# Optimization experiments

Measured on AMD Instinct MI355X. Metric: run time of the kernel, lower is better.

Reference implementation:

```python
import jax, jax.numpy as jnp
import numpy as np
import math

B, DM, H, W = 2, 96, 64, 64
DI, N, R, K = 192, 16, 6, 8


def _ln(x, w, b):
    mu = jnp.mean(x, axis=-1, keepdims=True)
    var = jnp.var(x, axis=-1, keepdims=True)
    return (x - mu) / jnp.sqrt(var + 1e-5) * w + b


def _conv2d(x, w, b, groups=1):
    y = jax.lax.conv_general_dilated(x, w, (1, 1), 'SAME',
                                     dimension_numbers=('NCHW', 'OIHW', 'NCHW'),
                                     feature_group_count=groups)
    return y + b[None, :, None, None]


def setup_inputs() -> dict:
    key = jax.random.key(0)
    ks = jax.random.split(key, 16)
    f32 = jnp.float32
    rn = lambda k, s, sc=0.02: jax.random.normal(k, s, dtype=f32) * sc
    dt = jnp.exp(jax.random.uniform(ks[11], (K, DI), dtype=f32)
                 * (math.log(0.1) - math.log(0.001)) + math.log(0.001))
    dt_bias = dt + jnp.log(-jnp.expm1(-dt))  # inverse softplus
    return dict(
        feat_m1=jax.random.normal(ks[0], (B, DM, H, W), f32),
        feat_m2=jax.random.normal(ks[1], (B, DM, H, W), f32),
        ln1_w=jnp.ones(DM, f32), ln1_b=jnp.zeros(DM, f32),
        ln2_w=jnp.ones(DM, f32), ln2_b=jnp.zeros(DM, f32),
        in_proj_m1_w=rn(ks[2], (2 * DI, DM)),
        in_proj_m2_w=rn(ks[3], (2 * DI, DM)),
        conv_m1_w=rn(ks[4], (DI, 1, 3, 3), 0.1), conv_m1_b=jnp.zeros(DI, f32),
        conv_m2_w=rn(ks[5], (DI, 1, 3, 3), 0.1), conv_m2_b=jnp.zeros(DI, f32),
        x_proj_weight=rn(ks[6], (K, R + 2 * N, DI)),
        dt_projs_weight=rn(ks[7], (K, DI, R), R ** -0.5),
        dt_projs_bias=dt_bias,
        A_logs=jnp.log(jnp.tile(jnp.arange(1, N + 1, dtype=f32)[None], (K * DI, 1))),
        Ds=jnp.ones(K * DI, f32),
        out_norm_w=jnp.ones(DI, f32), out_norm_b=jnp.zeros(DI, f32),
        cc0_w=rn(ks[8], (DI, 2, 3, 3), 0.1), cc0_b=jnp.zeros(DI, f32),
        cc1_w=rn(ks[9], (DI, 1, 3, 3), 0.1), cc1_b=jnp.zeros(DI, f32),
        cc2_w=rn(ks[10], (DM, DI, 1, 1), 0.05), cc2_b=jnp.zeros(DM, f32),
    )


def reference(feat_m1, feat_m2, ln1_w, ln1_b, ln2_w, ln2_b,
              in_proj_m1_w, in_proj_m2_w, conv_m1_w, conv_m1_b,
              conv_m2_w, conv_m2_b, x_proj_weight, dt_projs_weight,
              dt_projs_bias, A_logs, Ds, out_norm_w, out_norm_b,
              cc0_w, cc0_b, cc1_w, cc1_b, cc2_w, cc2_b):
    silu = jax.nn.silu
    Bb, _, Hh, Ww = feat_m1.shape
    L = Hh * Ww

    def branch(feat, lw, lb, pw, cw, cb):
        f = _ln(feat.transpose(0, 2, 3, 1), lw, lb)        # [B,H,W,DM]
        xz = f @ pw.T                                      # [B,H,W,2*DI]
        x, z = jnp.split(xz, 2, axis=-1)
        z = silu(z.transpose(0, 3, 1, 2))                  # [B,DI,H,W]
        x = silu(_conv2d(x.transpose(0, 3, 1, 2), cw, cb, groups=cw.shape[0]))
        return x, z

    x1, z1 = branch(feat_m1, ln1_w, ln1_b, in_proj_m1_w, conv_m1_w, conv_m1_b)
    x2, z2 = branch(feat_m2, ln2_w, ln2_b, in_proj_m2_w, conv_m2_w, conv_m2_b)
    Di = x1.shape[1]

    # 4 directions x 2 modalities -> K=8 scan streams
    x_hwwh = jnp.stack([x1.reshape(Bb, Di, L), x2.reshape(Bb, Di, L),
                        x1.transpose(0, 1, 3, 2).reshape(Bb, Di, L),
                        x2.transpose(0, 1, 3, 2).reshape(Bb, Di, L)], axis=1)
    xs = jnp.concatenate([x_hwwh, jnp.flip(x_hwwh, axis=-1)], axis=1)  # [B,K,DI,L]
    Kk = xs.shape[1]

    x_dbl = jnp.einsum('bkdl,kcd->bkcl', xs, x_proj_weight)
    Rr, Nn = dt_projs_weight.shape[2], A_logs.shape[1]
    dts, Bs, Cs = jnp.split(x_dbl, [Rr, Rr + Nn], axis=2)
    dts = jnp.einsum('bkrl,kdr->bkdl', dts, dt_projs_weight)

    A = -jnp.exp(A_logs).reshape(Kk, Di, Nn)               # [K,DI,N]
    delta = jax.nn.softplus(dts + dt_projs_bias[None, :, :, None])

    us = jnp.moveaxis(xs, -1, 0)      # [L,B,K,DI]
    ds = jnp.moveaxis(delta, -1, 0)   # [L,B,K,DI]
    bs = jnp.moveaxis(Bs, -1, 0)      # [L,B,K,N]
    cs = jnp.moveaxis(Cs, -1, 0)      # [L,B,K,N]

    def step(h, inp):
        u_t, d_t, b_t, c_t = inp
        h = jnp.exp(d_t[..., None] * A) * h + (d_t * u_t)[..., None] * b_t[:, :, None, :]
        return h, jnp.einsum('bkdn,bkn->bkd', h, c_t)

    h0 = jnp.zeros((Bb, Kk, Di, Nn), xs.dtype)
    _, ys = jax.lax.scan(step, h0, (us, ds, bs, cs))
    out_y = jnp.moveaxis(ys, 0, -1) + Ds.reshape(Kk, Di)[None, :, :, None] * xs  # [B,K,DI,L]

    inv_y = jnp.flip(out_y[:, 4:], axis=-1)

    def wh(t):  # undo transposed raster order
        return t.reshape(Bb, 2, Di, Ww, Hh).transpose(0, 1, 2, 4, 3).reshape(Bb, 2, Di, L)

    wh_y = wh(out_y[:, 2:4])
    invwh_y = wh(inv_y[:, 2:4])
    y = (out_y[:, 0] + inv_y[:, 0] + wh_y[:, 0] + invwh_y[:, 0]
         + out_y[:, 1] + inv_y[:, 1] + wh_y[:, 1] + invwh_y[:, 1])  # [B,DI,L]

    y = _ln(y.transpose(0, 2, 1), out_norm_w, out_norm_b).reshape(Bb, Hh, Ww, Di)
    yc = y.transpose(0, 3, 1, 2)
    y_fus = jnp.concatenate([yc * z1, yc * z2], axis=1)    # [B,2*DI,H,W]
    y_fus = silu(_conv2d(y_fus, cc0_w, cc0_b, groups=Di))
    y_fus = silu(_conv2d(y_fus, cc1_w, cc1_b, groups=Di))
    y_fus = _conv2d(y_fus, cc2_w, cc2_b, groups=1)
    return y_fus + feat_m1 + feat_m2
```

## Files before the change

### kernel.cpp

```cpp
#include <hip/hip_runtime.h>
#include <math.h>

#define Bq 2
#define DMq 96
#define Lq 4096
#define DIq 192
#define Nq 16
#define Rq 6
#define Kq 8
#define Cq 38
#define NCH 128
#define CHL 32

typedef _Float16 f16x2 __attribute__((ext_vector_type(2)));

#if defined(__has_builtin)
#if __has_builtin(__builtin_amdgcn_fdot2)
#define HAVE_FDOT2 1
#endif
#endif

__device__ __forceinline__ float fdot2_(f16x2 a, f16x2 b, float c) {
#ifdef HAVE_FDOT2
  return __builtin_amdgcn_fdot2(a, b, c, false);
#else
  return c + (float)a.x * (float)b.x + (float)a.y * (float)b.y;
#endif
}

__device__ __forceinline__ f16x2 pkrtz(float a, float b) {
#if defined(__has_builtin) && __has_builtin(__builtin_amdgcn_cvt_pkrtz)
  auto r = __builtin_amdgcn_cvt_pkrtz(a, b);
  return *(f16x2*)&r;
#else
  return (f16x2){(_Float16)a, (_Float16)b};
#endif
}

__device__ __forceinline__ f16x2 u2h(unsigned u) {
  union { unsigned u; f16x2 h; } v; v.u = u; return v.h;
}
__device__ __forceinline__ unsigned h2u(f16x2 h) {
  union { unsigned u; f16x2 h; } v; v.h = h; return v.u;
}

__device__ __forceinline__ float sigmoidf_(float x) { return 1.f / (1.f + __expf(-x)); }

__global__ __launch_bounds__(256) void kprep(
    const float* __restrict__ pw1, const float* __restrict__ pw2,
    const float* __restrict__ ln1w, const float* __restrict__ ln1b,
    const float* __restrict__ ln2w, const float* __restrict__ ln2b,
    const float* __restrict__ xpw, const float* __restrict__ w2,
    _Float16* __restrict__ pw1h, _Float16* __restrict__ pw2h,
    _Float16* __restrict__ xpwh, _Float16* __restrict__ w2h,
    float* __restrict__ PQ) {
  int r = blockIdx.x * 256 + threadIdx.x;
  if (r < 768) {
    int br = r >= 384;
    int c = r - br * 384;
    const float* pw = br ? pw2 : pw1;
    const float* lw = br ? ln2w : ln1w;
    const float* lb = br ? ln2b : ln1b;
    _Float16* dst = br ? pw2h : pw1h;
    float P = 0.f, Q = 0.f;
    for (int cc = 0; cc < DMq; ++cc) {
      float w = pw[c * DMq + cc];
      P += w * lb[cc];
      Q += w * lw[cc];
      dst[c * DMq + cc] = (_Float16)(w * lw[cc]);
    }
    PQ[br * 768 + 2 * c] = P;
    PQ[br * 768 + 2 * c + 1] = Q;
  } else if (r < 768 + 304) {
    int rr = r - 768;
    for (int d = 0; d < DIq; ++d) xpwh[rr * DIq + d] = (_Float16)xpw[rr * DIq + d];
  } else if (r < 768 + 304 + 96) {
    int rr = r - 1072;
    for (int d = 0; d < DIq; ++d) w2h[rr * DIq + d] = (_Float16)w2[rr * DIq + d];
  }
}

__global__ __launch_bounds__(512, 2) void k1_branch(
    const float* __restrict__ feat1, const float* __restrict__ feat2,
    const _Float16* __restrict__ pw1h, const _Float16* __restrict__ pw2h,
    const float* __restrict__ PQ,
    _Float16* __restrict__ xpre1, _Float16* __restrict__ xpre2,
    _Float16* __restrict__ z1, _Float16* __restrict__ z2) {
  int blk = blockIdx.x;
  int cq = blk & 1;
  int tile = (blk >> 1) & 63;
  int b = (blk >> 7) & 1;
  int br = blk >> 8;
  int l0 = tile * 64;
  const float* feat = br ? feat2 : feat1;
  const f16x2* pwh = (const f16x2*)(br ? pw2h : pw1h);
  const float* pq = PQ + br * 768;
  _Float16* xpre = br ? xpre2 : xpre1;
  _Float16* zsil = br ? z2 : z1;
  int lane = threadIdx.x & 63;
  int wid = __builtin_amdgcn_readfirstlane(threadIdx.x >> 6);
  const float* fp = feat + (size_t)b * DMq * Lq + l0 + lane;
  f16x2 fr2[48];
  float s = 0.f, s2 = 0.f;
#pragma unroll
  for (int i = 0; i < 48; ++i) {
    float v0 = fp[(size_t)(2 * i) * Lq];
    float v1 = fp[(size_t)(2 * i + 1) * Lq];
    s += v0 + v1;
    s2 += v0 * v0 + v1 * v1;
    fr2[i] = (f16x2){(_Float16)v0, (_Float16)v1};
  }
  float mu = s * (1.f / DMq);
  float var = s2 * (1.f / DMq) - mu * mu;
  float rs = rsqrtf(var + 1e-5f);
  int cbase = cq * 192 + wid * 24;
  for (int g = 0; g < 6; ++g) {
    int c = cbase + g * 4;
    const f16x2* w0 = pwh + (size_t)c * 48;
    float a0 = 0.f, a1 = 0.f, a2 = 0.f, a3 = 0.f;
#pragma unroll
    for (int i = 0; i < 48; ++i) {
      f16x2 v = fr2[i];
      a0 = fdot2_(v, w0[i], a0);
      a1 = fdot2_(v, w0[48 + i], a1);
      a2 = fdot2_(v, w0[96 + i], a2);
      a3 = fdot2_(v, w0[144 + i], a3);
    }
    float acc[4] = {a0, a1, a2, a3};
#pragma unroll
    for (int q = 0; q < 4; ++q) {
      int c2 = c + q;
      float out = rs * acc[q] - rs * mu * pq[2 * c2 + 1] + pq[2 * c2];
      if (c2 < DIq) {
        xpre[(size_t)(b * DIq + c2) * Lq + l0 + lane] = (_Float16)out;
      } else {
        zsil[(size_t)(b * DIq + (c2 - DIq)) * Lq + l0 + lane] =
            (_Float16)(out * sigmoidf_(out));
      }
    }
  }
}

__global__ __launch_bounds__(256) void k2_dwconv(
    const _Float16* __restrict__ xpre1, const _Float16* __restrict__ xpre2,
    const float* __restrict__ cw1, const float* __restrict__ cb1,
    const float* __restrict__ cw2, const float* __restrict__ cb2,
    _Float16* __restrict__ xsh) {
  int blk = blockIdx.x;
  int mod = blk >= 384;
  int r = blk - mod * 384;
  int strip = r & 31;
  int dg = (r >> 5) % 6;
  int b = r / 192;
  const _Float16* xpre = mod ? xpre2 : xpre1;
  const float* cw = mod ? cw2 : cw1;
  const float* cb = mod ? cb2 : cb1;
  int d0 = dg * 32;
  int h0 = strip * 2;
  __shared__ float in_s[4][64][33];
  int tid = threadIdx.x;
  const _Float16* src = xpre + (size_t)(b * DIq + d0) * Lq;
  for (int i = tid; i < 4 * 64 * 32; i += 256) {
    int w = i & 63;
    int t = i >> 6;
    int dd = t & 31;
    int rr = t >> 5;
    int row = h0 + rr - 1;
    float v = 0.f;
    if (row >= 0 && row < 64) v = (float)src[(size_t)dd * Lq + row * 64 + w];
    in_s[rr][w][dd] = v;
  }
  __syncthreads();
  int dd = tid & 31;
  float w9[9];
#pragma unroll
  for (int i = 0; i < 9; i++) w9[i] = cw[(d0 + dd) * 9 + i];
  float bias = cb[d0 + dd];
  _Float16* dst = xsh + (size_t)(b * 2 + mod) * Lq * DIq + d0 + dd;
  for (int i = tid; i < 2 * 64 * 32; i += 256) {
    int w = (i >> 5) & 63;
    int hh = i >> 11;
    float acc = bias;
#pragma unroll
    for (int dh = 0; dh < 3; dh++) {
#pragma unroll
      for (int dw = 0; dw < 3; dw++) {
        int ww = w + dw - 1;
        if (ww < 0 || ww > 63) continue;
        acc += in_s[hh + dh][ww][dd] * w9[dh * 3 + dw];
      }
    }
    float v = acc * sigmoidf_(acc);
    dst[((size_t)(h0 + hh) * 64 + w) * DIq] = (_Float16)v;
  }
}

__global__ __launch_bounds__(512, 2) void k3_proj(
    const _Float16* __restrict__ xsh, const _Float16* __restrict__ xpwh,
    unsigned* __restrict__ dtBu, unsigned* __restrict__ Ccu) {
  int blk = blockIdx.x;
  int tile = blk & 63;
  int kp = (blk >> 6) & 3;
  int b = blk >> 8;
  int mod = kp & 1;
  bool tr = kp >= 2;
  int tid = threadIdx.x;
  int lane = tid & 63;
  int wid = __builtin_amdgcn_readfirstlane(tid >> 6);
  int halfk = wid >> 2;
  int chq = wid & 3;
  int kk = kp + halfk * 4;
  int chb = chq * 10;
  __shared__ unsigned osu[2][64][25];
  if (chq == 0) { osu[halfk][lane][6] = 0u; osu[halfk][lane][7] = 0u; }
  int p = tr ? (lane * 64 + tile) : (tile * 64 + lane);
  const _Float16* xp = xsh + (size_t)(b * 2 + mod) * Lq * DIq + (size_t)p * DIq;
  float acc[10];
#pragma unroll
  for (int g = 0; g < 10; ++g) acc[g] = 0.f;
  for (int chunk = 0; chunk < 2; ++chunk) {
    f16x2 fr2[48];
    const uint4* xq = (const uint4*)(xp + chunk * 96);
#pragma unroll
    for (int i = 0; i < 12; ++i) {
      uint4 v = xq[i];
      fr2[4 * i] = u2h(v.x); fr2[4 * i + 1] = u2h(v.y);
      fr2[4 * i + 2] = u2h(v.z); fr2[4 * i + 3] = u2h(v.w);
    }
#pragma unroll
    for (int g = 0; g < 10; ++g) {
      int c = chb + g;
      int cr = (c <= 37) ? c : 37;
      const f16x2* w0 = (const f16x2*)(xpwh + ((size_t)kk * Cq + cr) * DIq) + chunk * 48;
      float a = acc[g];
#pragma unroll
      for (int i = 0; i < 48; ++i) a = fdot2_(fr2[i], w0[i], a);
      acc[g] = a;
    }
  }
#pragma unroll
  for (int g = 0; g < 10; g += 2) {
    int c = chb + g;
    if (c >= Cq) break;
    if (c < 6) {
      osu[halfk][lane][c] = __float_as_uint(acc[g]);
      osu[halfk][lane][c + 1] = __float_as_uint(acc[g + 1]);
    } else {
      int word = (c < 22) ? (8 + ((c - 6) >> 1)) : (16 + ((c - 22) >> 1));
      f16x2 pk = pkrtz(acc[g], acc[g + 1]);
      osu[halfk][lane][word] = h2u(pk);
    }
  }
  __syncthreads();
  for (int i = tid; i < 2 * 64 * 16; i += 512) {
    int hk = i >> 10;
    int rem = i & 1023;
    int jr = rem >> 4, slot = rem & 15;
    int kk2 = kp + hk * 4;
    int l = hk ? (4095 - tile * 64 - jr) : (tile * 64 + jr);
    dtBu[((size_t)(b * Kq + kk2) * Lq + l) * 16 + slot] = osu[hk][jr][slot];
  }
  for (int i = tid; i < 2 * 64 * 8; i += 512) {
    int hk = i >> 9;
    int rem = i & 511;
    int jr = rem >> 3, slot = rem & 7;
    int kk2 = kp + hk * 4;
    int l = hk ? (4095 - tile * 64 - jr) : (tile * 64 + jr);
    Ccu[((size_t)(b * Kq + kk2) * Lq + l) * 8 + slot] = osu[hk][jr][16 + slot];
  }
}

#define PREAMBLE(Q0, Q1, U)                                               \
  float a = bias + __uint_as_float(Q0.x) * wr[0] +                        \
            __uint_as_float(Q0.y) * wr[1] + __uint_as_float(Q0.z) * wr[2] + \
            __uint_as_float(Q0.w) * wr[3] + __uint_as_float(Q1.x) * wr[4] + \
            __uint_as_float(Q1.y) * wr[5];                                \
  float E_ = __expf(-fabsf(a));                                           \
  float dt = fmaxf(a, 0.f) + __logf(1.f + E_);                            \
  float du = dt * (U);                                                    \
  float e1f = __expf(-dt);                                                \
  float e2f = e1f * e1f;                                                  \
  f16x2 P1 = pkrtz(e1f, e2f);                                             \
  f16x2 Dp = pkrtz(e2f, e2f);                                             \
  f16x2 du2 = pkrtz(du, du);                                              \
  f16x2 pe1 = P1 * Dp, pe2 = pe1 * Dp, pe3 = pe2 * Dp, pe4 = pe3 * Dp,   \
        pe5 = pe4 * Dp, pe6 = pe5 * Dp, pe7 = pe6 * Dp;

#define HUPDATE(Q2, Q3)                                                   \
  hp0 = P1 * hp0 + du2 * u2h(Q2.x); hp1 = pe1 * hp1 + du2 * u2h(Q2.y);    \
  hp2 = pe2 * hp2 + du2 * u2h(Q2.z); hp3 = pe3 * hp3 + du2 * u2h(Q2.w);   \
  hp4 = pe4 * hp4 + du2 * u2h(Q3.x); hp5 = pe5 * hp5 + du2 * u2h(Q3.y);   \
  hp6 = pe6 * hp6 + du2 * u2h(Q3.z); hp7 = pe7 * hp7 + du2 * u2h(Q3.w);

#define STEPA(Q0, Q1, Q2, Q3, U) {                                        \
  PREAMBLE(Q0, Q1, U)                                                     \
  sdt += dt;                                                              \
  HUPDATE(Q2, Q3) }

#define STEPC(Q0, Q1, Q2, Q3, Q4, Q5, U, J) {                             \
  PREAMBLE(Q0, Q1, U)                                                     \
  HUPDATE(Q2, Q3)                                                         \
  float yv = 0.f;                                                         \
  yv = fdot2_(hp0, u2h(Q4.x), yv); yv = fdot2_(hp1, u2h(Q4.y), yv);       \
  yv = fdot2_(hp2, u2h(Q4.z), yv); yv = fdot2_(hp3, u2h(Q4.w), yv);       \
  yv = fdot2_(hp4, u2h(Q5.x), yv); yv = fdot2_(hp5, u2h(Q5.y), yv);       \
  yv = fdot2_(hp6, u2h(Q5.z), yv); yv = fdot2_(hp7, u2h(Q5.w), yv);       \
  yp[(size_t)(J) * DIq] = (_Float16)(yv + Dv * (U)); }

#define LD4(pfx, J) { const uint4* _q = sp + (size_t)(J) * 4;             \
  pfx##0 = _q[0]; pfx##1 = _q[1]; pfx##2 = _q[2]; pfx##3 = _q[3]; }

#define LD6C(pfx, J) { const uint4* _q = sp + (size_t)(J) * 4;            \
  pfx##0 = _q[0]; pfx##1 = _q[1]; pfx##2 = _q[2]; pfx##3 = _q[3];         \
  const uint4* _c = cp + (size_t)(J) * 2;                                 \
  pfx##4 = _c[0]; pfx##5 = _c[1]; }

__device__ __forceinline__ int canonpos_(int l, bool rev, bool tr) {
  int q = rev ? 4095 - l : l;
  return tr ? (((q & 63) << 6) | (q >> 6)) : q;
}

__global__ __launch_bounds__(192, 6) void k4a_local(
    const _Float16* __restrict__ xsh, const unsigned* __restrict__ dtBu,
    const float* __restrict__ dtw, const float* __restrict__ dtb,
    float* __restrict__ sumdt, _Float16* __restrict__ hendh) {
  int blk = blockIdx.x;
  int c = blk & 127, k = (blk >> 7) & 7, b = blk >> 10;
  int m = k & 3, mod = m & 1;
  bool rev = k >= 4, tr = m >= 2;
  int tid = threadIdx.x;
  int d = tid;
  __shared__ _Float16 uld[CHL][200];
  int p0 = canonpos_(c * CHL, rev, tr);
  int s = canonpos_(c * CHL + 1, rev, tr) - p0;
  const _Float16* uplane = xsh + (size_t)(b * 2 + mod) * Lq * DIq;
  const uint4* sp = (const uint4*)dtBu + ((size_t)(b * Kq + k) * Lq + c * CHL) * 4;
  for (int i = tid; i < CHL * 24; i += 192) {
    int j = i / 24, w = i - j * 24;
    const uint4* urow = (const uint4*)(uplane + (size_t)(p0 + s * j) * DIq);
    ((uint4*)&uld[j][0])[w] = urow[w];
  }
  __syncthreads();
  float wr[Rq];
#pragma unroll
  for (int r = 0; r < Rq; r++) wr[r] = dtw[(k * DIq + d) * Rq + r];
  float bias = dtb[k * DIq + d];
  f16x2 hz = (f16x2){(_Float16)0.f, (_Float16)0.f};
  f16x2 hp0 = hz, hp1 = hz, hp2 = hz, hp3 = hz, hp4 = hz, hp5 = hz, hp6 = hz, hp7 = hz;
  float sdt = 0.f;
  uint4 qa0, qa1, qa2, qa3, qb0, qb1, qb2, qb3;
  LD4(qa, 0)
  for (int jj = 0; jj < CHL; jj += 2) {
    LD4(qb, jj + 1)
    {
      float u0 = (float)uld[jj][d];
      STEPA(qa0, qa1, qa2, qa3, u0)
    }
    if (jj + 2 < CHL) LD4(qa, jj + 2)
    {
      float u1 = (float)uld[jj + 1][d];
      STEPA(qb0, qb1, qb2, qb3, u1)
    }
  }
  size_t cb = ((size_t)(b * Kq + k) * NCH + c) * DIq + d;
  sumdt[cb] = sdt;
  uint4* hv = (uint4*)(hendh + cb * Nq);
  hv[0] = make_uint4(h2u(hp0), h2u(hp1), h2u(hp2), h2u(hp3));
  hv[1] = make_uint4(h2u(hp4), h2u(hp5), h2u(hp6), h2u(hp7));
}

__global__ __launch_bounds__(256) void k4b_chain(
    const float* __restrict__ A_logs, const float* __restrict__ sumdt,
    _Float16* __restrict__ hendh) {
  int idx = blockIdx.x * 256 + threadIdx.x;
  int n = idx & 15;
  int dk = idx >> 4;
  int d = dk % DIq;
  int kb = dk / DIq;
  int k = kb & 7, b = kb >> 3;
  float A2 = -__expf(A_logs[(size_t)(k * DIq + d) * Nq + n]) * 1.44269504088896f;
  size_t basecb = ((size_t)(b * Kq + k) * NCH) * DIq + d;
  _Float16* hp = hendh + basecb * Nq + n;
  const float* sp2 = sumdt + basecb;
  const size_t HS = (size_t)DIq * Nq;
  float h = 0.f;
  float he = (float)hp[0], sd = sp2[0];
  for (int c = 0; c < NCH; ++c) {
    float he_n = 0.f, sd_n = 0.f;
    if (c < NCH - 1) {
      he_n = (float)hp[(size_t)(c + 1) * HS];
      sd_n = sp2[(size_t)(c + 1) * DIq];
    }
    hp[(size_t)c * HS] = (_Float16)h;
    h = exp2f(A2 * sd) * h + he;
    he = he_n; sd = sd_n;
  }
}

__global__ __launch_bounds__(192, 6) void k4c_out(
    const _Float16* __restrict__ xsh, const unsigned* __restrict__ dtBu,
    const unsigned* __restrict__ Ccu, const float* __restrict__ dtw,
    const float* __restrict__ dtb, const float* __restrict__ Ds,
    const _Float16* __restrict__ h0h, _Float16* __restrict__ ydirc) {
  int blk = blockIdx.x;
  int c = blk & 127, k = (blk >> 7) & 7, b = blk >> 10;
  int m = k & 3, mod = m & 1;
  bool rev = k >= 4, tr = m >= 2;
  int tid = threadIdx.x;
  int d = tid;
  __shared__ _Float16 uld[CHL][200];
  int p0 = canonpos_(c * CHL, rev, tr);
  int s = canonpos_(c * CHL + 1, rev, tr) - p0;
  const _Float16* uplane = xsh + (size_t)(b * 2 + mod) * Lq * DIq;
  const uint4* sp = (const uint4*)dtBu + ((size_t)(b * Kq + k) * Lq + c * CHL) * 4;
  const uint4* cp = (const uint4*)Ccu + ((size_t)(b * Kq + k) * Lq + c * CHL) * 2;
  for (int i = tid; i < CHL * 24; i += 192) {
    int j = i / 24, w = i - j * 24;
    const uint4* urow = (const uint4*)(uplane + (size_t)(p0 + s * j) * DIq);
    ((uint4*)&uld[j][0])[w] = urow[w];
  }
  __syncthreads();
  float wr[Rq];
#pragma unroll
  for (int r = 0; r < Rq; r++) wr[r] = dtw[(k * DIq + d) * Rq + r];
  float bias = dtb[k * DIq + d];
  float Dv = Ds[k * DIq + d];
  size_t cb = ((size_t)(b * Kq + k) * NCH + c) * DIq + d;
  const uint4* h0v = (const uint4*)(h0h + cb * Nq);
  uint4 ha = h0v[0], hb = h0v[1];
  f16x2 hp0 = u2h(ha.x), hp1 = u2h(ha.y), hp2 = u2h(ha.z), hp3 = u2h(ha.w);
  f16x2 hp4 = u2h(hb.x), hp5 = u2h(hb.y), hp6 = u2h(hb.z), hp7 = u2h(hb.w);
  _Float16* yp = ydirc + ((size_t)(b * Kq + k) * Lq) * DIq + d;
  uint4 qa0, qa1, qa2, qa3, qa4, qa5, qb0, qb1, qb2, qb3, qb4, qb5;
  LD6C(qa, 0)
  int p = p0;
  for (int jj = 0; jj < CHL; jj += 2) {
    LD6C(qb, jj + 1)
    {
      float u0 = (float)uld[jj][d];
      STEPC(qa0, qa1, qa2, qa3, qa4, qa5, u0, p)
    }
    if (jj + 2 < CHL) LD6C(qa, jj + 2)
    {
      float u1 = (float)uld[jj + 1][d];
      STEPC(qb0, qb1, qb2, qb3, qb4, qb5, u1, p + s)
    }
    p += 2 * s;
  }
}

__global__ __launch_bounds__(256) void kml(
    const _Float16* __restrict__ ydirc, const float* __restrict__ onw,
    const float* __restrict__ onb, _Float16* __restrict__ ych) {
  int blk = blockIdx.x;
  int wc = blk & 3;
  int h = (blk >> 2) & 63;
  int b = blk >> 8;
  int pix0 = h * 64 + wc * 16;
  __shared__ float acc[DIq][17];
  __shared__ float ps[16][17], ps2[16][17];
  __shared__ float mu[16], rs[16];
  int tid = threadIdx.x;
  const _Float16* base = ydirc + (size_t)b * Kq * Lq * DIq;
  const size_t SS = (size_t)Lq * DIq;
  for (int i = tid; i < 16 * 24; i += 256) {
    int c4 = i % 24, ww = i / 24;
    size_t off = (size_t)(pix0 + ww) * DIq + c4 * 8;
    float sum[8] = {0.f, 0.f, 0.f, 0.f, 0.f, 0.f, 0.f, 0.f};
#pragma unroll
    for (int k = 0; k < 8; ++k) {
      uint4 v = *(const uint4*)(base + (size_t)k * SS + off);
      f16x2 a0 = u2h(v.x), a1 = u2h(v.y), a2 = u2h(v.z), a3 = u2h(v.w);
      sum[0] += (float)a0.x; sum[1] += (float)a0.y;
      sum[2] += (float)a1.x; sum[3] += (float)a1.y;
      sum[4] += (float)a2.x; sum[5] += (float)a2.y;
      sum[6] += (float)a3.x; sum[7] += (float)a3.y;
    }
#pragma unroll
    for (int q = 0; q < 8; ++q) acc[c4 * 8 + q][ww] = sum[q];
  }
  __syncthreads();
  {
    int px = tid & 15, sg = tid >> 4;
    float s = 0.f, s2 = 0.f;
    for (int d = sg * 12; d < sg * 12 + 12; ++d) {
      float v = acc[d][px]; s += v; s2 += v * v;
    }
    ps[sg][px] = s; ps2[sg][px] = s2;
  }
  __syncthreads();
  if (tid < 16) {
    float s = 0.f, s2 = 0.f;
    for (int sg = 0; sg < 16; ++sg) { s += ps[sg][tid]; s2 += ps2[sg][tid]; }
    float mm = s * (1.f / DIq);
    float var = s2 * (1.f / DIq) - mm * mm;
    mu[tid] = mm;
    rs[tid] = rsqrtf(var + 1e-5f);
  }
  __syncthreads();
  for (int i = tid; i < DIq * 16; i += 256) {
    int ww = i & 15, d = i >> 4;
    float val = (acc[d][ww] - mu[ww]) * rs[ww] * onw[d] + onb[d];
    ych[(size_t)(b * DIq + d) * Lq + pix0 + ww] = (_Float16)val;
  }
}

__global__ __launch_bounds__(256) void k67_fused(
    const _Float16* __restrict__ ych, const _Float16* __restrict__ z1,
    const _Float16* __restrict__ z2, const float* __restrict__ w0,
    const float* __restrict__ b0, const float* __restrict__ w1c,
    const float* __restrict__ b1c, _Float16* __restrict__ t1h) {
  int blk = blockIdx.x;
  int strip = blk & 3;
  int g = (blk >> 2) % DIq;
  int b = blk / (4 * DIq);
  int h0 = strip * 16;
  int pb = h0 - 2;
  int c0 = 2 * g;
  const _Float16* zz = (c0 < DIq) ? z1 : z2;
  int cc0i = c0 % DIq, cc1i = (c0 + 1) % DIq;
  __shared__ float p0[20][64], p1[20][64];
  __shared__ float c0s[18][64];
  int tid = threadIdx.x;
  const _Float16* ycb = ych + (size_t)b * DIq * Lq;
  const _Float16* zb = zz + (size_t)b * DIq * Lq;
  for (int i = tid; i < 20 * 64; i += 256) {
    int r = i >> 6, w = i & 63;
    int row = pb + r;
    float v0 = 0.f, v1 = 0.f;
    if (row >= 0 && row < 64) {
      size_t o0 = (size_t)cc0i * Lq + row * 64 + w;
      size_t o1 = (size_t)cc1i * Lq + row * 64 + w;
      v0 = (float)ycb[o0] * (float)zb[o0];
      v1 = (float)ycb[o1] * (float)zb[o1];
    }
    p0[r][w] = v0; p1[r][w] = v1;
  }
  __syncthreads();
  float wa[9], wb[9];
#pragma unroll
  for (int i = 0; i < 9; i++) {
    wa[i] = w0[(size_t)(g * 2 + 0) * 9 + i];
    wb[i] = w0[(size_t)(g * 2 + 1) * 9 + i];
  }
  float bias0 = b0[g];
  for (int i = tid; i < 18 * 64; i += 256) {
    int rr = i >> 6, w = i & 63;
    int ho = h0 - 1 + rr;
    float acc = bias0;
#pragma unroll
    for (int dh = 0; dh < 3; dh++) {
#pragma unroll
      for (int dw = 0; dw < 3; dw++) {
        int ww = w + dw - 1;
        if (ww < 0 || ww > 63) continue;
        acc += p0[rr + dh][ww] * wa[dh * 3 + dw] + p1[rr + dh][ww] * wb[dh * 3 + dw];
      }
    }
    c0s[rr][w] = (ho >= 0 && ho < 64) ? acc * sigmoidf_(acc) : 0.f;
  }
  __syncthreads();
  float w9[9];
#pragma unroll
  for (int i = 0; i < 9; i++) w9[i] = w1c[g * 9 + i];
  float bias1 = b1c[g];
  for (int i = tid; i < 16 * 64; i += 256) {
    int hh = i >> 6, w = i & 63;
    float acc = bias1;
#pragma unroll
    for (int dh = 0; dh < 3; dh++) {
#pragma unroll
      for (int dw = 0; dw < 3; dw++) {
        int ww = w + dw - 1;
        if (ww < 0 || ww > 63) continue;
        acc += c0s[hh + dh][ww] * w9[dh * 3 + dw];
      }
    }
    t1h[(size_t)(b * DIq + g) * Lq + (h0 + hh) * 64 + w] =
        (_Float16)(acc * sigmoidf_(acc));
  }
}

__global__ __launch_bounds__(256) void k8_cc2(
    const _Float16* __restrict__ t1h, const _Float16* __restrict__ w2h,
    const float* __restrict__ b2, const float* __restrict__ f1,
    const float* __restrict__ f2, float* __restrict__ out) {
  int blk = blockIdx.x;
  int b = blk >> 8;
  int l0 = (blk & 255) << 4;
  __shared__ f16x2 hs[96][17];
  int tid = threadIdx.x;
  for (int i = tid; i < 96 * 16; i += 256) {
    int cp = i >> 4, j = i & 15;
    hs[cp][j] = (f16x2){t1h[(size_t)(b * DIq + 2 * cp) * Lq + l0 + j],
                        t1h[(size_t)(b * DIq + 2 * cp + 1) * Lq + l0 + j]};
  }
  __syncthreads();
  int j = tid & 15, mg = tid >> 4;
  for (int pass = 0; pass < 2; ++pass) {
    int mo = pass * 48 + mg * 3;
    const f16x2* wr = (const f16x2*)w2h + (size_t)mo * 96;
    float a0 = b2[mo], a1 = b2[mo + 1], a2 = b2[mo + 2];
#pragma unroll
    for (int cp = 0; cp < 96; ++cp) {
      f16x2 v = hs[cp][j];
      a0 = fdot2_(v, wr[cp], a0);
      a1 = fdot2_(v, wr[96 + cp], a1);
      a2 = fdot2_(v, wr[192 + cp], a2);
    }
    float acc[3] = {a0, a1, a2};
#pragma unroll
    for (int q = 0; q < 3; ++q) {
      size_t idx = (size_t)(b * DMq + mo + q) * Lq + l0 + j;
      out[idx] = acc[q] + f1[idx] + f2[idx];
    }
  }
}

extern "C" void kernel_launch(void* const* d_in, const int* in_sizes, int n_in,
                              void* d_out, int out_size, void* d_ws, size_t ws_size,
                              hipStream_t stream) {
  const float* feat1 = (const float*)d_in[0];
  const float* feat2 = (const float*)d_in[1];
  const float* ln1w = (const float*)d_in[2];
  const float* ln1b = (const float*)d_in[3];
  const float* ln2w = (const float*)d_in[4];
  const float* ln2b = (const float*)d_in[5];
  const float* pw1 = (const float*)d_in[6];
  const float* pw2 = (const float*)d_in[7];
  const float* cw1 = (const float*)d_in[8];
  const float* cb1 = (const float*)d_in[9];
  const float* cw2 = (const float*)d_in[10];
  const float* cb2 = (const float*)d_in[11];
  const float* xpw = (const float*)d_in[12];
  const float* dtw = (const float*)d_in[13];
  const float* dtb = (const float*)d_in[14];
  const float* A_logs = (const float*)d_in[15];
  const float* Ds = (const float*)d_in[16];
  const float* onw = (const float*)d_in[17];
  const float* onb = (const float*)d_in[18];
  const float* w0 = (const float*)d_in[19];
  const float* b0 = (const float*)d_in[20];
  const float* w1c = (const float*)d_in[21];
  const float* b1c = (const float*)d_in[22];
  const float* w2 = (const float*)d_in[23];
  const float* b2 = (const float*)d_in[24];

  float* W = (float*)d_ws;
  const size_t PL = (size_t)Bq * DIq * Lq;
  _Float16* xsh   = (_Float16*)(W + 0);
  _Float16* z1h   = (_Float16*)(W + PL);
  _Float16* z2h   = (_Float16*)(W + PL + PL / 2);
  float* dtB      = W + 2 * PL;
  float* Cc       = dtB + 1048576;
  float* sumdt    = Cc + 524288;
  _Float16* hendh = (_Float16*)(sumdt + 393216);
  _Float16* ydirc = (_Float16*)(sumdt + 393216 + 2 * PL);
  float* after    = sumdt + 393216 + 6 * PL;
  _Float16* ych   = (_Float16*)after;
  _Float16* xpre1 = (_Float16*)(after + PL / 2);
  _Float16* xpre2 = (_Float16*)(after + PL);
  _Float16* t1h   = (_Float16*)(after + 3 * PL / 2);
  float* tail     = after + 2 * PL;
  _Float16* pw1h = (_Float16*)tail;
  _Float16* pw2h = pw1h + 36864;
  _Float16* xpwh = pw2h + 36864;
  _Float16* w2h  = xpwh + 58368;
  float* PQ = tail + 75264;

  kprep<<<5, 256, 0, stream>>>(pw1, pw2, ln1w, ln1b, ln2w, ln2b, xpw, w2,
                               pw1h, pw2h, xpwh, w2h, PQ);
  k1_branch<<<512, 512, 0, stream>>>(feat1, feat2, pw1h, pw2h, PQ,
                                     xpre1, xpre2, z1h, z2h);
  k2_dwconv<<<768, 256, 0, stream>>>(xpre1, xpre2, cw1, cb1, cw2, cb2, xsh);
  k3_proj<<<512, 512, 0, stream>>>(xsh, xpwh, (unsigned*)dtB, (unsigned*)Cc);
  k4a_local<<<2048, 192, 0, stream>>>(xsh, (const unsigned*)dtB, dtw, dtb,
                                      sumdt, hendh);
  k4b_chain<<<192, 256, 0, stream>>>(A_logs, sumdt, hendh);
  k4c_out<<<2048, 192, 0, stream>>>(xsh, (const unsigned*)dtB,
                                    (const unsigned*)Cc, dtw, dtb, Ds,
                                    hendh, ydirc);
  kml<<<512, 256, 0, stream>>>(ydirc, onw, onb, ych);
  k67_fused<<<1536, 256, 0, stream>>>(ych, z1h, z2h, w0, b0, w1c, b1c, t1h);
  k8_cc2<<<512, 256, 0, stream>>>(t1h, w2h, b2, feat1, feat2, (float*)d_out);
}
```

Measured before the change: 208.6 us.

## Rewrite x_proj kernel to use MFMA 16x16x32 f16 matrix instructions

Replaces the per-thread fdot2 implementation of the x_proj projection with a kernel that stages a 64-position tile of activations in shared memory and computes the 76x64 output tile with MFMA 16x16x32 f16 instructions. Wave 0 handles an extra fifth M-tile. Results go to an fp32 shared buffer and are packed into the dtB/C layouts during the store loop. The block shrinks to 256 threads. The aim is to move the dot-product work onto the matrix cores, at the cost of uneven wave work and a larger shared-memory footprint.

```diff
diff --git a/kernel.cpp b/kernel.cpp
--- a/kernel.cpp
+++ b/kernel.cpp
@@ -13,6 +13,8 @@
 #define CHL 32
 
 typedef _Float16 f16x2 __attribute__((ext_vector_type(2)));
+typedef _Float16 f16x8 __attribute__((ext_vector_type(8)));
+typedef float f32x4 __attribute__((ext_vector_type(4)));
 
 #if defined(__has_builtin)
 #if __has_builtin(__builtin_amdgcn_fdot2)
@@ -195,7 +197,7 @@
   }
 }
 
-__global__ __launch_bounds__(512, 2) void k3_proj(
+__global__ __launch_bounds__(256, 2) void k3_mfma(
     const _Float16* __restrict__ xsh, const _Float16* __restrict__ xpwh,
     unsigned* __restrict__ dtBu, unsigned* __restrict__ Ccu) {
   int blk = blockIdx.x;
@@ -206,67 +208,78 @@
   bool tr = kp >= 2;
   int tid = threadIdx.x;
   int lane = tid & 63;
-  int wid = __builtin_amdgcn_readfirstlane(tid >> 6);
-  int halfk = wid >> 2;
-  int chq = wid & 3;
-  int kk = kp + halfk * 4;
-  int chb = chq * 10;
-  __shared__ unsigned osu[2][64][25];
-  if (chq == 0) { osu[halfk][lane][6] = 0u; osu[halfk][lane][7] = 0u; }
-  int p = tr ? (lane * 64 + tile) : (tile * 64 + lane);
-  const _Float16* xp = xsh + (size_t)(b * 2 + mod) * Lq * DIq + (size_t)p * DIq;
-  float acc[10];
-#pragma unroll
-  for (int g = 0; g < 10; ++g) acc[g] = 0.f;
-  for (int chunk = 0; chunk < 2; ++chunk) {
-    f16x2 fr2[48];
-    const uint4* xq = (const uint4*)(xp + chunk * 96);
-#pragma unroll
-    for (int i = 0; i < 12; ++i) {
-      uint4 v = xq[i];
-      fr2[4 * i] = u2h(v.x); fr2[4 * i + 1] = u2h(v.y);
-      fr2[4 * i + 2] = u2h(v.z); fr2[4 * i + 3] = u2h(v.w);
-    }
-#pragma unroll
-    for (int g = 0; g < 10; ++g) {
-      int c = chb + g;
-      int cr = (c <= 37) ? c : 37;
-      const f16x2* w0 = (const f16x2*)(xpwh + ((size_t)kk * Cq + cr) * DIq) + chunk * 48;
-      float a = acc[g];
-#pragma unroll
-      for (int i = 0; i < 48; ++i) a = fdot2_(fr2[i], w0[i], a);
-      acc[g] = a;
-    }
-  }
-#pragma unroll
-  for (int g = 0; g < 10; g += 2) {
-    int c = chb + g;
-    if (c >= Cq) break;
-    if (c < 6) {
-      osu[halfk][lane][c] = __float_as_uint(acc[g]);
-      osu[halfk][lane][c + 1] = __float_as_uint(acc[g + 1]);
-    } else {
-      int word = (c < 22) ? (8 + ((c - 6) >> 1)) : (16 + ((c - 22) >> 1));
-      f16x2 pk = pkrtz(acc[g], acc[g + 1]);
-      osu[halfk][lane][word] = h2u(pk);
-    }
-  }
-  __syncthreads();
-  for (int i = tid; i < 2 * 64 * 16; i += 512) {
+  int wave = __builtin_amdgcn_readfirstlane(tid >> 6);
+  __shared__ _Float16 xls[64][200];
+  __shared__ float osu[80][64];
+  const _Float16* xp = xsh + (size_t)(b * 2 + mod) * Lq * DIq;
+  for (int i = tid; i < 64 * 24; i += 256) {
+    int j = i / 24, w = i - j * 24;
+    int p = tr ? (j * 64 + tile) : (tile * 64 + j);
+    ((uint4*)&xls[j][0])[w] = ((const uint4*)(xp + (size_t)p * DIq))[w];
+  }
+  __syncthreads();
+  int row16 = lane & 15;
+  int kgrp = lane >> 4;
+  for (int mi = 0; mi < 2; ++mi) {
+    if (mi == 1 && wave != 0) break;
+    int mt = (mi == 0) ? wave : 4;
+    f16x8 af[6];
+    {
+      int row = mt * 16 + row16;
+      int hk = row >= 38;
+      int cc = row - 38 * hk;
+      if (cc > 37) cc = 37;
+      int kkA = kp + hk * 4;
+      const _Float16* wbase = xpwh + ((size_t)kkA * Cq + cc) * DIq + kgrp * 8;
+#pragma unroll
+      for (int ks = 0; ks < 6; ++ks)
+        af[ks] = *(const f16x8*)(wbase + ks * 32);
+    }
+#pragma unroll
+    for (int nt = 0; nt < 4; ++nt) {
+      f32x4 acc = {0.f, 0.f, 0.f, 0.f};
+#pragma unroll
+      for (int ks = 0; ks < 6; ++ks) {
+        f16x8 bf = *(const f16x8*)(&xls[nt * 16 + row16][ks * 32 + kgrp * 8]);
+        acc = __builtin_amdgcn_mfma_f32_16x16x32_f16(af[ks], bf, acc, 0, 0, 0);
+      }
+      int ocol = nt * 16 + row16;
+#pragma unroll
+      for (int r = 0; r < 4; ++r) {
+        int orow = mt * 16 + kgrp * 4 + r;
+        if (orow < 76) osu[orow][ocol] = acc[r];
+      }
+    }
+  }
+  __syncthreads();
+  for (int i = tid; i < 2 * 64 * 16; i += 256) {
     int hk = i >> 10;
     int rem = i & 1023;
     int jr = rem >> 4, slot = rem & 15;
+    int rb = hk * 38;
+    unsigned val;
+    if (slot < 6) {
+      val = __float_as_uint(osu[rb + slot][jr]);
+    } else if (slot < 8) {
+      val = 0u;
+    } else {
+      int c = 6 + 2 * (slot - 8);
+      val = h2u(pkrtz(osu[rb + c][jr], osu[rb + c + 1][jr]));
+    }
     int kk2 = kp + hk * 4;
     int l = hk ? (4095 - tile * 64 - jr) : (tile * 64 + jr);
-    dtBu[((size_t)(b * Kq + kk2) * Lq + l) * 16 + slot] = osu[hk][jr][slot];
-  }
-  for (int i = tid; i < 2 * 64 * 8; i += 512) {
+    dtBu[((size_t)(b * Kq + kk2) * Lq + l) * 16 + slot] = val;
+  }
+  for (int i = tid; i < 2 * 64 * 8; i += 256) {
     int hk = i >> 9;
     int rem = i & 511;
     int jr = rem >> 3, slot = rem & 7;
+    int rb = hk * 38;
+    int c = 22 + 2 * slot;
+    unsigned val = h2u(pkrtz(osu[rb + c][jr], osu[rb + c + 1][jr]));
     int kk2 = kp + hk * 4;
     int l = hk ? (4095 - tile * 64 - jr) : (tile * 64 + jr);
-    Ccu[((size_t)(b * Kq + kk2) * Lq + l) * 8 + slot] = osu[hk][jr][16 + slot];
+    Ccu[((size_t)(b * Kq + kk2) * Lq + l) * 8 + slot] = val;
   }
 }
 
@@ -673,7 +686,7 @@
   k1_branch<<<512, 512, 0, stream>>>(feat1, feat2, pw1h, pw2h, PQ,
                                      xpre1, xpre2, z1h, z2h);
   k2_dwconv<<<768, 256, 0, stream>>>(xpre1, xpre2, cw1, cb1, cw2, cb2, xsh);
-  k3_proj<<<512, 512, 0, stream>>>(xsh, xpwh, (unsigned*)dtB, (unsigned*)Cc);
+  k3_mfma<<<512, 256, 0, stream>>>(xsh, xpwh, (unsigned*)dtB, (unsigned*)Cc);
   k4a_local<<<2048, 192, 0, stream>>>(xsh, (const unsigned*)dtB, dtw, dtb,
                                       sumdt, hendh);
   k4b_chain<<<192, 256, 0, stream>>>(A_logs, sumdt, hendh);
```

Measured after the change: 198.1 us. -5.0%, faster.
